# Optimization experiments

Hardware: AMD Instinct MI355X
Metric: run time of the kernel (lower is better)

The kernel has to match this reference:

```python
import jax, jax.numpy as jnp
import numpy as np

B, S, D, H, F, R = 4, 128, 512, 8, 2048, 8
DH = D // H
THRESH = 0.1  # hardcoded in the torch module


def _ln(x, g, b):
    m = x.mean(-1, keepdims=True)
    v = ((x - m) ** 2).mean(-1, keepdims=True)
    return (x - m) * jax.lax.rsqrt(v + 1e-5) * g + b


def setup_inputs() -> dict:
    key = jax.random.key(0)
    ks = jax.random.split(key, 12)
    w = lambda k, shape, std: jax.random.normal(k, shape, jnp.float32) * std
    s = 1.0 / np.sqrt(D)
    qk_std = 2.0 / np.sqrt(D)  # peaky attention so adjacency threshold fires
    return {
        "x": jax.random.normal(ks[0], (B, S, D), jnp.float32),
        "ln1_g": jnp.ones(D, jnp.float32), "ln1_b": jnp.zeros(D, jnp.float32),
        "wq": w(ks[1], (D, D), qk_std), "bq": jnp.zeros(D, jnp.float32),
        "wk": w(ks[2], (D, D), qk_std), "bk": jnp.zeros(D, jnp.float32),
        "wv": w(ks[3], (D, D), s), "bv": jnp.zeros(D, jnp.float32),
        "wo": w(ks[4], (D, D), s), "bo": jnp.zeros(D, jnp.float32),
        "w1": w(ks[5], (D, F), s), "b1": jnp.zeros(F, jnp.float32),
        "w2": w(ks[6], (F, D), 1.0 / np.sqrt(F)), "b2": jnp.zeros(D, jnp.float32),
        "rc_w1": w(ks[7], (2 * D, D), 1.0 / np.sqrt(2 * D)), "rc_b1": jnp.zeros(D, jnp.float32),
        "rc_w2": w(ks[8], (D, R), s), "rc_b2": jnp.zeros(R, jnp.float32),
        "kg_w": w(ks[9], (R, D, D), s),
        "s2n_w": w(ks[10], (D, D), s), "s2n_b": jnp.zeros(D, jnp.float32),
        "ln2_g": jnp.ones(D, jnp.float32), "ln2_b": jnp.zeros(D, jnp.float32),
    }


def reference(x, ln1_g, ln1_b, wq, bq, wk, bk, wv, bv, wo, bo,
              w1, b1, w2, b2, rc_w1, rc_b1, rc_w2, rc_b2,
              kg_w, s2n_w, s2n_b, ln2_g, ln2_b):
    # pre-norm attention
    xn = _ln(x, ln1_g, ln1_b)
    q = (xn @ wq + bq).reshape(B, S, H, DH)
    k = (xn @ wk + bk).reshape(B, S, H, DH)
    v = (xn @ wv + bv).reshape(B, S, H, DH)
    scores = jnp.einsum('bihd,bjhd->bhij', q, k) / np.sqrt(DH)
    attn = jax.nn.softmax(scores, axis=-1)                  # [B,H,S,S]
    ctx = jnp.einsum('bhij,bjhd->bihd', attn, v).reshape(B, S, D)
    attn_out = ctx @ wo + bo
    # FFN -> neural_understanding (no residual, as in source)
    nu = jax.nn.relu(attn_out @ w1 + b1) @ w2 + b2          # [B,S,D]
    # dynamic edge extraction, expressed as a dense mask (jit-safe)
    am = attn.mean(axis=1)                                  # [B,S,S]
    adj = (am > THRESH) & (~jnp.eye(S, dtype=bool))         # u != v
    # relation classifier on every (u,v) pair; mask selects real edges
    a_part = nu @ rc_w1[:D]                                 # concept1 half
    b_part = nu @ rc_w1[D:]                                 # concept2 half
    h = jax.nn.relu(a_part[:, :, None, :] + b_part[:, None, :, :] + rc_b1)  # [B,S,S,D]
    logits = h @ rc_w2 + rc_b2                              # [B,S,S,R]
    pred = jnp.argmax(logits, axis=-1)
    valid = adj & (pred != 0)                               # relation 0 == NONE
    oh = jax.nn.one_hot(pred, R, dtype=nu.dtype) * valid[..., None].astype(nu.dtype)
    # RGCN-style knowledge graph conv: message u -> v with per-relation weight
    transformed = jnp.einsum('bud,rde->bure', nu, kg_w)     # [B,S,R,D]
    agg = jnp.einsum('buvr,bure->bve', oh, transformed)     # [B,S,D]
    reasoned = nu + agg
    neural_result = reasoned @ s2n_w + s2n_b
    out = _ln(x + neural_result, ln2_g, ln2_b)
    return out
```

## Files before the change

kernel.cpp:

```cpp
#include <hip/hip_runtime.h>
#include <hip/hip_bf16.h>

#define B_ 4
#define S_ 128
#define D_ 512
#define H_ 8
#define DH_ 64
#define F_ 2048
#define R_ 8
#define BS_ (B_ * S_)
#define BSD_ (BS_ * D_)
#define E_ 262144

typedef __attribute__((ext_vector_type(8))) short short8;
typedef __attribute__((ext_vector_type(4))) float f32x4;
typedef __attribute__((ext_vector_type(4))) unsigned short ushort4v;

__device__ __forceinline__ void split2(float a, unsigned short& h, unsigned short& l) {
    unsigned u = __float_as_uint(a);
    unsigned hr = (u + 0x7FFFu + ((u >> 16) & 1u)) >> 16;
    h = (unsigned short)hr;
    float lo = a - __uint_as_float(hr << 16);
    unsigned u2 = __float_as_uint(lo);
    l = (unsigned short)((u2 + 0x7FFFu + ((u2 >> 16) & 1u)) >> 16);
}

#define RP 40

struct GemmLds {
    unsigned short A[2][2][64][RP];
    unsigned short B[2][2][64][RP];
};

struct TDesc { const float* s; unsigned short* h; unsigned short* l; int K; int N; int off; };
struct TPack { TDesc d[10]; };

__global__ void prep_kernel(TPack p, int nt, const float* __restrict__ x,
                            const float* __restrict__ g, const float* __restrict__ be,
                            unsigned short* __restrict__ xh, unsigned short* __restrict__ xl) {
    __shared__ float tr[32][33];
    __shared__ float red[256];
    int bid = blockIdx.x;
    if (bid < nt) {
        int wi = 0;
#pragma unroll
        for (int i = 1; i < 10; ++i) if (bid >= p.d[i].off) wi = i;
        const TDesc dd = p.d[wi];
        int t = bid - dd.off;
        int ntk = dd.K / 32;
        int tk = t % ntk, tn = t / ntk;
        int k0 = tk * 32, n0 = tn * 32;
        int col = threadIdx.x & 31, rg = threadIdx.x >> 5;
#pragma unroll
        for (int i = 0; i < 4; ++i) {
            int row = rg * 4 + i;
            tr[row][col] = dd.s[(size_t)(k0 + row) * dd.N + n0 + col];
        }
        __syncthreads();
#pragma unroll
        for (int i = 0; i < 4; ++i) {
            int n = n0 + rg * 4 + i;
            int k = k0 + col;
            unsigned short h, l;
            split2(tr[col][rg * 4 + i], h, l);
            dd.h[(size_t)n * dd.K + k] = h;
            dd.l[(size_t)n * dd.K + k] = l;
        }
    } else {
        int row = bid - nt;
        int t = threadIdx.x;
        const float* xr = x + (size_t)row * D_;
        float v0 = xr[t], v1 = xr[t + 256];
        red[t] = v0 + v1;
        __syncthreads();
        for (int off = 128; off > 0; off >>= 1) { if (t < off) red[t] += red[t + off]; __syncthreads(); }
        float mean = red[0] * (1.0f / D_);
        __syncthreads();
        float d0 = v0 - mean, d1 = v1 - mean;
        red[t] = d0 * d0 + d1 * d1;
        __syncthreads();
        for (int off = 128; off > 0; off >>= 1) { if (t < off) red[t] += red[t + off]; __syncthreads(); }
        float rs = rsqrtf(red[0] * (1.0f / D_) + 1e-5f);
        float o0 = d0 * rs * g[t] + be[t];
        float o1 = d1 * rs * g[t + 256] + be[t + 256];
        unsigned short h, l;
        split2(o0, h, l); xh[(size_t)row * D_ + t] = h;       xl[(size_t)row * D_ + t] = l;
        split2(o1, h, l); xh[(size_t)row * D_ + t + 256] = h; xl[(size_t)row * D_ + t + 256] = l;
    }
}

__device__ __forceinline__ void mgemm_core(const unsigned short* __restrict__ Ath,
                                           const unsigned short* __restrict__ Atl,
                                           const unsigned short* __restrict__ Bth,
                                           const unsigned short* __restrict__ Btl,
                                           int K, int rowBase, int colBase,
                                           int kStart, int nsteps,
                                           f32x4 acc[2][2], GemmLds* L) {
    int tid = threadIdx.x;
    int w = tid >> 6, lane = tid & 63;
    int lm = lane & 15, quad = lane >> 4;
    int wm = (w & 1) * 32, wn = (w >> 1) * 32;
    int rS = tid >> 2, kcS = (tid & 3) * 8;
    size_t aoff = (size_t)(rowBase + rS) * K + kStart + kcS;
    size_t boff = (size_t)(colBase + rS) * K + kStart + kcS;
    short8 rah = *(const short8*)&Ath[aoff];
    short8 ral = *(const short8*)&Atl[aoff];
    short8 rbh = *(const short8*)&Bth[boff];
    short8 rbl = *(const short8*)&Btl[boff];
    for (int s = 0; s < nsteps; ++s) {
        int p = s & 1;
        *(short8*)&L->A[p][0][rS][kcS] = rah;
        *(short8*)&L->A[p][1][rS][kcS] = ral;
        *(short8*)&L->B[p][0][rS][kcS] = rbh;
        *(short8*)&L->B[p][1][rS][kcS] = rbl;
        __syncthreads();
        if (s + 1 < nsteps) {
            size_t ao = aoff + (size_t)(s + 1) * 32;
            size_t bo = boff + (size_t)(s + 1) * 32;
            rah = *(const short8*)&Ath[ao];
            ral = *(const short8*)&Atl[ao];
            rbh = *(const short8*)&Bth[bo];
            rbl = *(const short8*)&Btl[bo];
        }
        short8 ah[2], al[2], bh[2], bl[2];
#pragma unroll
        for (int t = 0; t < 2; ++t) {
            ah[t] = *(const short8*)&L->A[p][0][wm + t * 16 + lm][quad * 8];
            al[t] = *(const short8*)&L->A[p][1][wm + t * 16 + lm][quad * 8];
            bh[t] = *(const short8*)&L->B[p][0][wn + t * 16 + lm][quad * 8];
            bl[t] = *(const short8*)&L->B[p][1][wn + t * 16 + lm][quad * 8];
        }
#pragma unroll
        for (int tm = 0; tm < 2; ++tm)
#pragma unroll
            for (int tn = 0; tn < 2; ++tn) {
                acc[tm][tn] = __builtin_amdgcn_mfma_f32_16x16x32_bf16(ah[tm], bh[tn], acc[tm][tn], 0, 0, 0);
                acc[tm][tn] = __builtin_amdgcn_mfma_f32_16x16x32_bf16(ah[tm], bl[tn], acc[tm][tn], 0, 0, 0);
                acc[tm][tn] = __builtin_amdgcn_mfma_f32_16x16x32_bf16(al[tm], bh[tn], acc[tm][tn], 0, 0, 0);
            }
    }
}

__global__ __launch_bounds__(256) void mgemm_kernel(const unsigned short* __restrict__ Ath,
                                                    const unsigned short* __restrict__ Atl,
                                                    const unsigned short* __restrict__ Bth,
                                                    const unsigned short* __restrict__ Btl,
                                                    const float* __restrict__ bias,
                                                    float* __restrict__ Cf,
                                                    unsigned short* __restrict__ Ch,
                                                    unsigned short* __restrict__ Cl,
                                                    int N, int K, int relu) {
    __shared__ GemmLds L;
    int tid = threadIdx.x;
    int w = tid >> 6, lane = tid & 63;
    int lm = lane & 15, quad = lane >> 4;
    int wm = (w & 1) * 32, wn = (w >> 1) * 32;
    int rowBase = blockIdx.y * 64, colBase = blockIdx.x * 64;
    f32x4 acc[2][2] = {};
    mgemm_core(Ath, Atl, Bth, Btl, K, rowBase, colBase, 0, K / 32, acc, &L);
#pragma unroll
    for (int tm = 0; tm < 2; ++tm)
#pragma unroll
        for (int tn = 0; tn < 2; ++tn) {
            int col = colBase + wn + tn * 16 + lm;
            float bi = bias ? bias[col] : 0.f;
#pragma unroll
            for (int r = 0; r < 4; ++r) {
                int row = rowBase + wm + tm * 16 + quad * 4 + r;
                float v = acc[tm][tn][r] + bi;
                if (relu) v = fmaxf(v, 0.f);
                size_t o = (size_t)row * N + col;
                if (Cf) Cf[o] = v;
                if (Ch) {
                    unsigned short sh, sl;
                    split2(v, sh, sl);
                    Ch[o] = sh; Cl[o] = sl;
                }
            }
        }
}

__global__ __launch_bounds__(256) void mgemm_zw_kernel(const unsigned short* __restrict__ Ath,
                                                       const unsigned short* __restrict__ Atl,
                                                       const unsigned short* __restrict__ Bth,
                                                       const unsigned short* __restrict__ Btl,
                                                       const float* __restrict__ b0,
                                                       const float* __restrict__ b1,
                                                       const float* __restrict__ b2,
                                                       float* __restrict__ Cbase,
                                                       int M, int N, int K) {
    __shared__ GemmLds L;
    int z = blockIdx.z;
    const unsigned short* bth = Bth + (size_t)z * K * N;
    const unsigned short* btl = Btl + (size_t)z * K * N;
    const float* bias = (z == 0) ? b0 : (z == 1) ? b1 : b2;
    float* C = Cbase + (size_t)z * M * N;
    int tid = threadIdx.x;
    int w = tid >> 6, lane = tid & 63;
    int lm = lane & 15, quad = lane >> 4;
    int wm = (w & 1) * 32, wn = (w >> 1) * 32;
    int rowBase = blockIdx.y * 64, colBase = blockIdx.x * 64;
    f32x4 acc[2][2] = {};
    mgemm_core(Ath, Atl, bth, btl, K, rowBase, colBase, 0, K / 32, acc, &L);
#pragma unroll
    for (int tm = 0; tm < 2; ++tm)
#pragma unroll
        for (int tn = 0; tn < 2; ++tn) {
            int col = colBase + wn + tn * 16 + lm;
            float bi = bias ? bias[col] : 0.f;
#pragma unroll
            for (int r = 0; r < 4; ++r) {
                int row = rowBase + wm + tm * 16 + quad * 4 + r;
                C[(size_t)row * N + col] = acc[tm][tn][r] + bi;
            }
        }
}

__global__ __launch_bounds__(256) void mgemm_part_kernel(const unsigned short* __restrict__ Ath,
                                                         const unsigned short* __restrict__ Atl,
                                                         const unsigned short* __restrict__ Bth,
                                                         const unsigned short* __restrict__ Btl,
                                                         float* __restrict__ Cbase,
                                                         int M, int N, int K) {
    __shared__ GemmLds L;
    int ks = gridDim.z, z = blockIdx.z;
    int kLen = K / ks, kStart = z * kLen;
    float* C = Cbase + (size_t)z * M * N;
    int tid = threadIdx.x;
    int w = tid >> 6, lane = tid & 63;
    int lm = lane & 15, quad = lane >> 4;
    int wm = (w & 1) * 32, wn = (w >> 1) * 32;
    int rowBase = blockIdx.y * 64, colBase = blockIdx.x * 64;
    f32x4 acc[2][2] = {};
    mgemm_core(Ath, Atl, Bth, Btl, K, rowBase, colBase, kStart, kLen / 32, acc, &L);
#pragma unroll
    for (int tm = 0; tm < 2; ++tm)
#pragma unroll
        for (int tn = 0; tn < 2; ++tn) {
            int col = colBase + wn + tn * 16 + lm;
#pragma unroll
            for (int r = 0; r < 4; ++r) {
                int row = rowBase + wm + tm * 16 + quad * 4 + r;
                C[(size_t)row * N + col] = acc[tm][tn][r];
            }
        }
}

__global__ void reduce4_kernel(const float* __restrict__ part, const float* __restrict__ b2,
                               float* __restrict__ nu,
                               unsigned short* __restrict__ nh, unsigned short* __restrict__ nl) {
    int base = blockIdx.x * 1024 + threadIdx.x * 4;
    f32x4 s = *(const f32x4*)&b2[base & (D_ - 1)];
#pragma unroll
    for (int z = 0; z < 4; ++z) s += *(const f32x4*)&part[(size_t)z * BSD_ + base];
    *(f32x4*)&nu[base] = s;
    ushort4v hv, lv;
#pragma unroll
    for (int i = 0; i < 4; ++i) { unsigned short h, l; split2(s[i], h, l); hv[i] = h; lv[i] = l; }
    *(ushort4v*)&nh[base] = hv;
    *(ushort4v*)&nl[base] = lv;
}

__global__ void reduce8_kernel(const float* __restrict__ part, const float* __restrict__ nu,
                               unsigned short* __restrict__ rh, unsigned short* __restrict__ rl) {
    int base = blockIdx.x * 1024 + threadIdx.x * 4;
    f32x4 s = *(const f32x4*)&nu[base];
#pragma unroll
    for (int z = 0; z < 8; ++z) s += *(const f32x4*)&part[(size_t)z * BSD_ + base];
    ushort4v hv, lv;
#pragma unroll
    for (int i = 0; i < 4; ++i) { unsigned short h, l; split2(s[i], h, l); hv[i] = h; lv[i] = l; }
    *(ushort4v*)&rh[base] = hv;
    *(ushort4v*)&rl[base] = lv;
}

__global__ __launch_bounds__(512) void attn_fused_kernel(const float* __restrict__ q,
                                                         const float* __restrict__ k,
                                                         const float* __restrict__ v,
                                                         unsigned short* __restrict__ ch,
                                                         unsigned short* __restrict__ cl,
                                                         int* __restrict__ ecount,
                                                         int* __restrict__ elist) {
    __shared__ float qsm[H_][DH_];
    __shared__ float psm[H_][S_];
    int h = threadIdx.x >> 6, lane = threadIdx.x & 63;
    int blk = blockIdx.x;
    int i = blk & (S_ - 1);
    int b = blk >> 7;
    const float* qrow = q + (size_t)(b * S_ + i) * D_ + h * DH_;
    qsm[h][lane] = qrow[lane];
    __syncthreads();
    float s0 = 0.f, s1 = 0.f;
    const float* k0p = k + (size_t)(b * S_ + lane) * D_ + h * DH_;
    const float* k1p = k0p + (size_t)64 * D_;
#pragma unroll 8
    for (int d = 0; d < DH_; ++d) {
        float qd = qsm[h][d];
        s0 += qd * k0p[d];
        s1 += qd * k1p[d];
    }
    s0 *= 0.125f; s1 *= 0.125f;
    float m = fmaxf(s0, s1);
#pragma unroll
    for (int off = 32; off > 0; off >>= 1) m = fmaxf(m, __shfl_xor(m, off));
    float e0 = __expf(s0 - m), e1 = __expf(s1 - m);
    float sum = e0 + e1;
#pragma unroll
    for (int off = 32; off > 0; off >>= 1) sum += __shfl_xor(sum, off);
    float inv = 1.f / sum;
    psm[h][lane] = e0 * inv;
    psm[h][lane + 64] = e1 * inv;
    __syncthreads();
    if (threadIdx.x < S_) {
        int j = threadIdx.x;
        float s = 0.f;
#pragma unroll
        for (int hh = 0; hh < H_; ++hh) s += psm[hh][j];
        s *= (1.0f / H_);
        if (s > 0.1f && i != j) {
            int p = atomicAdd(ecount, 1);
            elist[p] = blk * S_ + j;
        }
    }
    const float* vbase = v + (size_t)b * S_ * D_ + h * DH_ + lane;
    float acc = 0.f;
    for (int j = 0; j < S_; ++j) acc += psm[h][j] * vbase[(size_t)j * D_];
    unsigned short sh, sl;
    split2(acc, sh, sl);
    size_t o = (size_t)(b * S_ + i) * D_ + h * DH_ + lane;
    ch[o] = sh; cl[o] = sl;
}

__global__ __launch_bounds__(64) void edge_kernel(const float* __restrict__ a_part,
                                                  const float* __restrict__ b_part,
                                                  const float* __restrict__ rc_b1,
                                                  const float* __restrict__ rc_w2,
                                                  const float* __restrict__ rc_b2,
                                                  const int* __restrict__ elist,
                                                  const int* __restrict__ ecount,
                                                  int* __restrict__ rel) {
    int lane = threadIdx.x;
    int n = *ecount;
    for (int e = blockIdx.x; e < n; e += gridDim.x) {
        int idx = elist[e];
        int vv = idx & (S_ - 1);
        int bu = idx >> 7;
        int u = bu & (S_ - 1);
        int b = bu >> 7;
        const float* ap = a_part + (size_t)(b * S_ + u) * D_;
        const float* bp = b_part + (size_t)(b * S_ + vv) * D_;
        float lp[R_];
#pragma unroll
        for (int r = 0; r < R_; ++r) lp[r] = 0.f;
#pragma unroll
        for (int jj = 0; jj < D_ / 64; ++jj) {
            int d = lane + jj * 64;
            float hv = fmaxf(ap[d] + bp[d] + rc_b1[d], 0.f);
#pragma unroll
            for (int r = 0; r < R_; ++r) lp[r] += hv * rc_w2[d * R_ + r];
        }
#pragma unroll
        for (int r = 0; r < R_; ++r) {
#pragma unroll
            for (int off = 32; off > 0; off >>= 1) lp[r] += __shfl_down(lp[r], off);
        }
        if (lane == 0) {
            float best = lp[0] + rc_b2[0];
            int bi = 0;
#pragma unroll
            for (int r = 1; r < R_; ++r) {
                float L = lp[r] + rc_b2[r];
                if (L > best) { best = L; bi = r; }
            }
            rel[idx] = bi;
        }
    }
}

__global__ __launch_bounds__(128) void mbuild_kernel(const float* __restrict__ nu,
                                                     const int* __restrict__ rel,
                                                     unsigned short* __restrict__ Mh,
                                                     unsigned short* __restrict__ Ml) {
    __shared__ float acc[R_ * D_];
    __shared__ int rl[S_];
    int blk = blockIdx.x;
    int vv = blk & (S_ - 1);
    int b = blk >> 7;
    int t = threadIdx.x;
    for (int i = t; i < R_ * D_; i += 128) acc[i] = 0.f;
    rl[t] = rel[((size_t)b * S_ + t) * S_ + vv];
    __syncthreads();
    for (int u = 0; u < S_; ++u) {
        int r = rl[u];
        if (r > 0) {
            const float* nurow = nu + (size_t)(b * S_ + u) * D_;
            float* arow = acc + r * D_;
#pragma unroll
            for (int jj = 0; jj < D_ / 128; ++jj) arow[t + jj * 128] += nurow[t + jj * 128];
        }
    }
    __syncthreads();
    unsigned short* Hrow = Mh + (size_t)blk * (R_ * D_);
    unsigned short* Lrow = Ml + (size_t)blk * (R_ * D_);
    for (int i = t; i < R_ * D_; i += 128) {
        unsigned short sh, sl;
        split2(acc[i], sh, sl);
        Hrow[i] = sh; Lrow[i] = sl;
    }
}

__global__ void ln2_kernel(const float* __restrict__ x, const float* __restrict__ y,
                           const float* __restrict__ g, const float* __restrict__ be,
                           float* __restrict__ out) {
    int row = blockIdx.x;
    int t = threadIdx.x;
    __shared__ float red[256];
    float v0 = x[row * D_ + t]       + y[row * D_ + t];
    float v1 = x[row * D_ + t + 256] + y[row * D_ + t + 256];
    red[t] = v0 + v1;
    __syncthreads();
    for (int off = 128; off > 0; off >>= 1) {
        if (t < off) red[t] += red[t + off];
        __syncthreads();
    }
    float mean = red[0] * (1.0f / D_);
    __syncthreads();
    float d0 = v0 - mean, d1 = v1 - mean;
    red[t] = d0 * d0 + d1 * d1;
    __syncthreads();
    for (int off = 128; off > 0; off >>= 1) {
        if (t < off) red[t] += red[t + off];
        __syncthreads();
    }
    float rs = rsqrtf(red[0] * (1.0f / D_) + 1e-5f);
    out[row * D_ + t]       = d0 * rs * g[t]       + be[t];
    out[row * D_ + t + 256] = d1 * rs * g[t + 256] + be[t + 256];
}

extern "C" void kernel_launch(void* const* d_in, const int* in_sizes, int n_in,
                              void* d_out, int out_size, void* d_ws, size_t ws_size,
                              hipStream_t stream) {
    const float* x     = (const float*)d_in[0];
    const float* ln1_g = (const float*)d_in[1];
    const float* ln1_b = (const float*)d_in[2];
    const float* wq    = (const float*)d_in[3];
    const float* bq    = (const float*)d_in[4];
    const float* wk    = (const float*)d_in[5];
    const float* bk    = (const float*)d_in[6];
    const float* wv    = (const float*)d_in[7];
    const float* bv    = (const float*)d_in[8];
    const float* wo    = (const float*)d_in[9];
    const float* bo    = (const float*)d_in[10];
    const float* w1    = (const float*)d_in[11];
    const float* b1    = (const float*)d_in[12];
    const float* w2    = (const float*)d_in[13];
    const float* b2    = (const float*)d_in[14];
    const float* rc_w1 = (const float*)d_in[15];
    const float* rc_b1 = (const float*)d_in[16];
    const float* rc_w2 = (const float*)d_in[17];
    const float* rc_b2 = (const float*)d_in[18];
    const float* kg_w  = (const float*)d_in[19];
    const float* s2n_w = (const float*)d_in[20];
    const float* s2n_b = (const float*)d_in[21];
    const float* ln2_g = (const float*)d_in[22];
    const float* ln2_b = (const float*)d_in[23];
    float* out = (float*)d_out;

    const int BS  = BS_;
    const int BSD = BSD_;

    unsigned short* wt = (unsigned short*)d_ws;
    unsigned short* qkv_h = wt;
    unsigned short* qkv_l = wt + 3 * E_;
    unsigned short* wo_h  = wt + 6 * E_;
    unsigned short* wo_l  = wt + 7 * E_;
    unsigned short* w1_h  = wt + 8 * E_;
    unsigned short* w1_l  = wt + 12 * E_;
    unsigned short* w2_h  = wt + 16 * E_;
    unsigned short* w2_l  = wt + 20 * E_;
    unsigned short* rc_h  = wt + 24 * E_;
    unsigned short* rc_l  = wt + 26 * E_;
    unsigned short* kg_h  = wt + 28 * E_;
    unsigned short* kg_l  = wt + 36 * E_;
    unsigned short* s2_h  = wt + 44 * E_;
    unsigned short* s2_l  = wt + 45 * E_;

    unsigned short* xn_h  = wt + 46 * E_;
    unsigned short* xn_l  = xn_h + BSD;
    unsigned short* ctx_h = xn_l + BSD;
    unsigned short* ctx_l = ctx_h + BSD;
    unsigned short* ao_h  = ctx_l + BSD;
    unsigned short* ao_l  = ao_h + BSD;
    unsigned short* hid_h = ao_l + BSD;
    unsigned short* hid_l = hid_h + (size_t)BS * F_;
    unsigned short* nu_h  = hid_l + (size_t)BS * F_;
    unsigned short* nu_l  = nu_h + BSD;
    unsigned short* mb_h  = nu_l + BSD;
    unsigned short* mb_l  = mb_h + (size_t)BS * R_ * D_;
    unsigned short* rs_h  = mb_l + (size_t)BS * R_ * D_;
    unsigned short* rs_l  = rs_h + BSD;

    float* fbase  = (float*)(rs_l + BSD);
    float* q      = fbase;
    float* v_     = q + 2 * BSD;
    float* apart  = q + 3 * BSD;
    float* nu     = apart + 2 * BSD;
    float* y      = nu + BSD;
    float* part4  = y + BSD;
    float* part8  = part4 + 4 * BSD;

    int* rel    = (int*)(part8 + 8 * BSD);
    int* ecount = rel + B_ * S_ * S_;
    int* elist  = ecount + 64;

    hipMemsetAsync(rel, 0, (size_t)(B_ * S_ * S_ + 64) * 4, stream);
    TPack tp;
    int off = 0;
    auto setd = [&](int i, const float* s, unsigned short* h, unsigned short* l, int K, int N) {
        tp.d[i] = TDesc{s, h, l, K, N, off};
        off += (K / 32) * (N / 32);
    };
    setd(0, wq, qkv_h,          qkv_l,          D_, D_);
    setd(1, wk, qkv_h + E_,     qkv_l + E_,     D_, D_);
    setd(2, wv, qkv_h + 2 * E_, qkv_l + 2 * E_, D_, D_);
    setd(3, wo, wo_h, wo_l, D_, D_);
    setd(4, w1, w1_h, w1_l, D_, F_);
    setd(5, w2, w2_h, w2_l, F_, D_);
    setd(6, rc_w1,            rc_h,      rc_l,      D_, D_);
    setd(7, rc_w1 + D_ * D_,  rc_h + E_, rc_l + E_, D_, D_);
    setd(8, kg_w, kg_h, kg_l, R_ * D_, D_);
    setd(9, s2n_w, s2_h, s2_l, D_, D_);
    hipLaunchKernelGGL(prep_kernel, dim3(off + BS), dim3(256), 0, stream, tp, off,
                       x, ln1_g, ln1_b, xn_h, xn_l);

    hipLaunchKernelGGL(mgemm_zw_kernel, dim3(D_ / 64, BS / 64, 3), dim3(256), 0, stream,
                       xn_h, xn_l, qkv_h, qkv_l, bq, bk, bv, q, BS, D_, D_);
    hipLaunchKernelGGL(attn_fused_kernel, dim3(BS), dim3(512), 0, stream,
                       q, q + BSD, v_, ctx_h, ctx_l, ecount, elist);
    hipLaunchKernelGGL(mgemm_kernel, dim3(D_ / 64, BS / 64), dim3(256), 0, stream,
                       ctx_h, ctx_l, wo_h, wo_l, bo, (float*)nullptr, ao_h, ao_l, D_, D_, 0);
    hipLaunchKernelGGL(mgemm_kernel, dim3(F_ / 64, BS / 64), dim3(256), 0, stream,
                       ao_h, ao_l, w1_h, w1_l, b1, (float*)nullptr, hid_h, hid_l, F_, D_, 1);
    hipLaunchKernelGGL(mgemm_part_kernel, dim3(D_ / 64, BS / 64, 4), dim3(256), 0, stream,
                       hid_h, hid_l, w2_h, w2_l, part4, BS, D_, F_);
    hipLaunchKernelGGL(reduce4_kernel, dim3(BSD / 1024), dim3(256), 0, stream,
                       part4, b2, nu, nu_h, nu_l);
    hipLaunchKernelGGL(mgemm_zw_kernel, dim3(D_ / 64, BS / 64, 2), dim3(256), 0, stream,
                       nu_h, nu_l, rc_h, rc_l, (const float*)nullptr, (const float*)nullptr,
                       (const float*)nullptr, apart, BS, D_, D_);
    hipLaunchKernelGGL(edge_kernel, dim3(256), dim3(64), 0, stream,
                       apart, apart + BSD, rc_b1, rc_w2, rc_b2, elist, ecount, rel);
    hipLaunchKernelGGL(mbuild_kernel, dim3(BS), dim3(128), 0, stream, nu, rel, mb_h, mb_l);
    hipLaunchKernelGGL(mgemm_part_kernel, dim3(D_ / 64, BS / 64, 8), dim3(256), 0, stream,
                       mb_h, mb_l, kg_h, kg_l, part8, BS, D_, R_ * D_);
    hipLaunchKernelGGL(reduce8_kernel, dim3(BSD / 1024), dim3(256), 0, stream,
                       part8, nu, rs_h, rs_l);
    hipLaunchKernelGGL(mgemm_kernel, dim3(D_ / 64, BS / 64), dim3(256), 0, stream,
                       rs_h, rs_l, s2_h, s2_l, s2n_b, y, (unsigned short*)nullptr,
                       (unsigned short*)nullptr, D_, D_, 0);
    hipLaunchKernelGGL(ln2_kernel, dim3(BS), dim3(256), 0, stream, x, y, ln2_g, ln2_b, out);
}
```

Before: 252.5 us.

## Load GEMM fragments directly from global memory and pack four edges per block

Measured after the change: 307.6 us. +21.8%, slower.

```diff
diff --git a/kernel.cpp b/kernel.cpp
--- a/kernel.cpp
+++ b/kernel.cpp
@@ -24,13 +24,6 @@
     unsigned u2 = __float_as_uint(lo);
     l = (unsigned short)((u2 + 0x7FFFu + ((u2 >> 16) & 1u)) >> 16);
 }
-
-#define RP 40
-
-struct GemmLds {
-    unsigned short A[2][2][64][RP];
-    unsigned short B[2][2][64][RP];
-};
 
 struct TDesc { const float* s; unsigned short* h; unsigned short* l; int K; int N; int off; };
 struct TPack { TDesc d[10]; };
@@ -95,40 +88,34 @@
                                            const unsigned short* __restrict__ Btl,
                                            int K, int rowBase, int colBase,
                                            int kStart, int nsteps,
-                                           f32x4 acc[2][2], GemmLds* L) {
+                                           f32x4 acc[2][2]) {
     int tid = threadIdx.x;
     int w = tid >> 6, lane = tid & 63;
     int lm = lane & 15, quad = lane >> 4;
     int wm = (w & 1) * 32, wn = (w >> 1) * 32;
-    int rS = tid >> 2, kcS = (tid & 3) * 8;
-    size_t aoff = (size_t)(rowBase + rS) * K + kStart + kcS;
-    size_t boff = (size_t)(colBase + rS) * K + kStart + kcS;
-    short8 rah = *(const short8*)&Ath[aoff];
-    short8 ral = *(const short8*)&Atl[aoff];
-    short8 rbh = *(const short8*)&Bth[boff];
-    short8 rbl = *(const short8*)&Btl[boff];
+    size_t aoff = (size_t)(rowBase + wm + lm) * K + kStart + quad * 8;
+    size_t boff = (size_t)(colBase + wn + lm) * K + kStart + quad * 8;
+    const size_t rstep = (size_t)16 * K;
+    short8 ah[2], al[2], bh[2], bl[2];
+#pragma unroll
+    for (int t = 0; t < 2; ++t) {
+        ah[t] = *(const short8*)&Ath[aoff + t * rstep];
+        al[t] = *(const short8*)&Atl[aoff + t * rstep];
+        bh[t] = *(const short8*)&Bth[boff + t * rstep];
+        bl[t] = *(const short8*)&Btl[boff + t * rstep];
+    }
     for (int s = 0; s < nsteps; ++s) {
-        int p = s & 1;
-        *(short8*)&L->A[p][0][rS][kcS] = rah;
-        *(short8*)&L->A[p][1][rS][kcS] = ral;
-        *(short8*)&L->B[p][0][rS][kcS] = rbh;
-        *(short8*)&L->B[p][1][rS][kcS] = rbl;
-        __syncthreads();
+        short8 nah[2], nal[2], nbh[2], nbl[2];
         if (s + 1 < nsteps) {
             size_t ao = aoff + (size_t)(s + 1) * 32;
             size_t bo = boff + (size_t)(s + 1) * 32;
-            rah = *(const short8*)&Ath[ao];
-            ral = *(const short8*)&Atl[ao];
-            rbh = *(const short8*)&Bth[bo];
-            rbl = *(const short8*)&Btl[bo];
-        }
-        short8 ah[2], al[2], bh[2], bl[2];
-#pragma unroll
-        for (int t = 0; t < 2; ++t) {
-            ah[t] = *(const short8*)&L->A[p][0][wm + t * 16 + lm][quad * 8];
-            al[t] = *(const short8*)&L->A[p][1][wm + t * 16 + lm][quad * 8];
-            bh[t] = *(const short8*)&L->B[p][0][wn + t * 16 + lm][quad * 8];
-            bl[t] = *(const short8*)&L->B[p][1][wn + t * 16 + lm][quad * 8];
+#pragma unroll
+            for (int t = 0; t < 2; ++t) {
+                nah[t] = *(const short8*)&Ath[ao + t * rstep];
+                nal[t] = *(const short8*)&Atl[ao + t * rstep];
+                nbh[t] = *(const short8*)&Bth[bo + t * rstep];
+                nbl[t] = *(const short8*)&Btl[bo + t * rstep];
+            }
         }
 #pragma unroll
         for (int tm = 0; tm < 2; ++tm)
@@ -138,6 +125,12 @@
                 acc[tm][tn] = __builtin_amdgcn_mfma_f32_16x16x32_bf16(ah[tm], bl[tn], acc[tm][tn], 0, 0, 0);
                 acc[tm][tn] = __builtin_amdgcn_mfma_f32_16x16x32_bf16(al[tm], bh[tn], acc[tm][tn], 0, 0, 0);
             }
+        if (s + 1 < nsteps) {
+#pragma unroll
+            for (int t = 0; t < 2; ++t) {
+                ah[t] = nah[t]; al[t] = nal[t]; bh[t] = nbh[t]; bl[t] = nbl[t];
+            }
+        }
     }
 }
 
@@ -150,14 +143,13 @@
                                                     unsigned short* __restrict__ Ch,
                                                     unsigned short* __restrict__ Cl,
                                                     int N, int K, int relu) {
-    __shared__ GemmLds L;
     int tid = threadIdx.x;
     int w = tid >> 6, lane = tid & 63;
     int lm = lane & 15, quad = lane >> 4;
     int wm = (w & 1) * 32, wn = (w >> 1) * 32;
     int rowBase = blockIdx.y * 64, colBase = blockIdx.x * 64;
     f32x4 acc[2][2] = {};
-    mgemm_core(Ath, Atl, Bth, Btl, K, rowBase, colBase, 0, K / 32, acc, &L);
+    mgemm_core(Ath, Atl, Bth, Btl, K, rowBase, colBase, 0, K / 32, acc);
 #pragma unroll
     for (int tm = 0; tm < 2; ++tm)
 #pragma unroll
@@ -189,7 +181,6 @@
                                                        const float* __restrict__ b2,
                                                        float* __restrict__ Cbase,
                                                        int M, int N, int K) {
-    __shared__ GemmLds L;
     int z = blockIdx.z;
     const unsigned short* bth = Bth + (size_t)z * K * N;
     const unsigned short* btl = Btl + (size_t)z * K * N;
@@ -201,7 +192,7 @@
     int wm = (w & 1) * 32, wn = (w >> 1) * 32;
     int rowBase = blockIdx.y * 64, colBase = blockIdx.x * 64;
     f32x4 acc[2][2] = {};
-    mgemm_core(Ath, Atl, bth, btl, K, rowBase, colBase, 0, K / 32, acc, &L);
+    mgemm_core(Ath, Atl, bth, btl, K, rowBase, colBase, 0, K / 32, acc);
 #pragma unroll
     for (int tm = 0; tm < 2; ++tm)
 #pragma unroll
@@ -222,7 +213,6 @@
                                                          const unsigned short* __restrict__ Btl,
                                                          float* __restrict__ Cbase,
                                                          int M, int N, int K) {
-    __shared__ GemmLds L;
     int ks = gridDim.z, z = blockIdx.z;
     int kLen = K / ks, kStart = z * kLen;
     float* C = Cbase + (size_t)z * M * N;
@@ -232,7 +222,7 @@
     int wm = (w & 1) * 32, wn = (w >> 1) * 32;
     int rowBase = blockIdx.y * 64, colBase = blockIdx.x * 64;
     f32x4 acc[2][2] = {};
-    mgemm_core(Ath, Atl, Bth, Btl, K, rowBase, colBase, kStart, kLen / 32, acc, &L);
+    mgemm_core(Ath, Atl, Bth, Btl, K, rowBase, colBase, kStart, kLen / 32, acc);
 #pragma unroll
     for (int tm = 0; tm < 2; ++tm)
 #pragma unroll
@@ -331,17 +321,17 @@
     ch[o] = sh; cl[o] = sl;
 }
 
-__global__ __launch_bounds__(64) void edge_kernel(const float* __restrict__ a_part,
-                                                  const float* __restrict__ b_part,
-                                                  const float* __restrict__ rc_b1,
-                                                  const float* __restrict__ rc_w2,
-                                                  const float* __restrict__ rc_b2,
-                                                  const int* __restrict__ elist,
-                                                  const int* __restrict__ ecount,
-                                                  int* __restrict__ rel) {
-    int lane = threadIdx.x;
+__global__ __launch_bounds__(256) void edge_kernel(const float* __restrict__ a_part,
+                                                   const float* __restrict__ b_part,
+                                                   const float* __restrict__ rc_b1,
+                                                   const float* __restrict__ rc_w2,
+                                                   const float* __restrict__ rc_b2,
+                                                   const int* __restrict__ elist,
+                                                   const int* __restrict__ ecount,
+                                                   int* __restrict__ rel) {
+    int w = threadIdx.x >> 6, lane = threadIdx.x & 63;
     int n = *ecount;
-    for (int e = blockIdx.x; e < n; e += gridDim.x) {
+    for (int e = blockIdx.x * 4 + w; e < n; e += gridDim.x * 4) {
         int idx = elist[e];
         int vv = idx & (S_ - 1);
         int bu = idx >> 7;
@@ -548,7 +538,7 @@
     hipLaunchKernelGGL(mgemm_zw_kernel, dim3(D_ / 64, BS / 64, 2), dim3(256), 0, stream,
                        nu_h, nu_l, rc_h, rc_l, (const float*)nullptr, (const float*)nullptr,
                        (const float*)nullptr, apart, BS, D_, D_);
-    hipLaunchKernelGGL(edge_kernel, dim3(256), dim3(64), 0, stream,
+    hipLaunchKernelGGL(edge_kernel, dim3(256), dim3(256), 0, stream,
                        apart, apart + BSD, rc_b1, rc_w2, rc_b2, elist, ecount, rel);
     hipLaunchKernelGGL(mbuild_kernel, dim3(BS), dim3(128), 0, stream, nu, rel, mb_h, mb_l);
     hipLaunchKernelGGL(mgemm_part_kernel, dim3(D_ / 64, BS / 64, 8), dim3(256), 0, stream,
```

## Load GEMM tiles directly to LDS and pack four edges per block

Applied to the files above, without the earlier changes.

Measured after the change: 251.3 us. Within noise of the previous version (-0.5%).

```diff
diff --git a/kernel.cpp b/kernel.cpp
--- a/kernel.cpp
+++ b/kernel.cpp
@@ -25,13 +25,6 @@
     l = (unsigned short)((u2 + 0x7FFFu + ((u2 >> 16) & 1u)) >> 16);
 }
 
-#define RP 40
-
-struct GemmLds {
-    unsigned short A[2][2][64][RP];
-    unsigned short B[2][2][64][RP];
-};
-
 struct TDesc { const float* s; unsigned short* h; unsigned short* l; int K; int N; int off; };
 struct TPack { TDesc d[10]; };
 
@@ -87,6 +80,17 @@
         split2(o0, h, l); xh[(size_t)row * D_ + t] = h;       xl[(size_t)row * D_ + t] = l;
         split2(o1, h, l); xh[(size_t)row * D_ + t + 256] = h; xl[(size_t)row * D_ + t + 256] = l;
     }
+}
+
+struct GemmLds {
+    unsigned short A[2][2][64][32];
+    unsigned short B[2][2][64][32];
+};
+
+__device__ __forceinline__ void gload16(const unsigned short* g, unsigned short* l) {
+    __builtin_amdgcn_global_load_lds(
+        (const __attribute__((address_space(1))) void*)g,
+        (__attribute__((address_space(3))) void*)l, 16, 0, 0);
 }
 
 __device__ __forceinline__ void mgemm_core(const unsigned short* __restrict__ Ath,
@@ -101,26 +105,24 @@
     int lm = lane & 15, quad = lane >> 4;
     int wm = (w & 1) * 32, wn = (w >> 1) * 32;
     int rS = tid >> 2, kcS = (tid & 3) * 8;
+    int wb = w * 512;
     size_t aoff = (size_t)(rowBase + rS) * K + kStart + kcS;
     size_t boff = (size_t)(colBase + rS) * K + kStart + kcS;
-    short8 rah = *(const short8*)&Ath[aoff];
-    short8 ral = *(const short8*)&Atl[aoff];
-    short8 rbh = *(const short8*)&Bth[boff];
-    short8 rbl = *(const short8*)&Btl[boff];
+    gload16(&Ath[aoff], &L->A[0][0][0][0] + wb);
+    gload16(&Atl[aoff], &L->A[0][1][0][0] + wb);
+    gload16(&Bth[boff], &L->B[0][0][0][0] + wb);
+    gload16(&Btl[boff], &L->B[0][1][0][0] + wb);
+    __syncthreads();
     for (int s = 0; s < nsteps; ++s) {
         int p = s & 1;
-        *(short8*)&L->A[p][0][rS][kcS] = rah;
-        *(short8*)&L->A[p][1][rS][kcS] = ral;
-        *(short8*)&L->B[p][0][rS][kcS] = rbh;
-        *(short8*)&L->B[p][1][rS][kcS] = rbl;
-        __syncthreads();
         if (s + 1 < nsteps) {
+            int pn = p ^ 1;
             size_t ao = aoff + (size_t)(s + 1) * 32;
             size_t bo = boff + (size_t)(s + 1) * 32;
-            rah = *(const short8*)&Ath[ao];
-            ral = *(const short8*)&Atl[ao];
-            rbh = *(const short8*)&Bth[bo];
-            rbl = *(const short8*)&Btl[bo];
+            gload16(&Ath[ao], &L->A[pn][0][0][0] + wb);
+            gload16(&Atl[ao], &L->A[pn][1][0][0] + wb);
+            gload16(&Bth[bo], &L->B[pn][0][0][0] + wb);
+            gload16(&Btl[bo], &L->B[pn][1][0][0] + wb);
         }
         short8 ah[2], al[2], bh[2], bl[2];
 #pragma unroll
@@ -138,6 +140,7 @@
                 acc[tm][tn] = __builtin_amdgcn_mfma_f32_16x16x32_bf16(ah[tm], bl[tn], acc[tm][tn], 0, 0, 0);
                 acc[tm][tn] = __builtin_amdgcn_mfma_f32_16x16x32_bf16(al[tm], bh[tn], acc[tm][tn], 0, 0, 0);
             }
+        __syncthreads();
     }
 }
 
@@ -331,17 +334,17 @@
     ch[o] = sh; cl[o] = sl;
 }
 
-__global__ __launch_bounds__(64) void edge_kernel(const float* __restrict__ a_part,
-                                                  const float* __restrict__ b_part,
-                                                  const float* __restrict__ rc_b1,
-                                                  const float* __restrict__ rc_w2,
-                                                  const float* __restrict__ rc_b2,
-                                                  const int* __restrict__ elist,
-                                                  const int* __restrict__ ecount,
-                                                  int* __restrict__ rel) {
-    int lane = threadIdx.x;
+__global__ __launch_bounds__(256) void edge_kernel(const float* __restrict__ a_part,
+                                                   const float* __restrict__ b_part,
+                                                   const float* __restrict__ rc_b1,
+                                                   const float* __restrict__ rc_w2,
+                                                   const float* __restrict__ rc_b2,
+                                                   const int* __restrict__ elist,
+                                                   const int* __restrict__ ecount,
+                                                   int* __restrict__ rel) {
+    int w = threadIdx.x >> 6, lane = threadIdx.x & 63;
     int n = *ecount;
-    for (int e = blockIdx.x; e < n; e += gridDim.x) {
+    for (int e = blockIdx.x * 4 + w; e < n; e += gridDim.x * 4) {
         int idx = elist[e];
         int vv = idx & (S_ - 1);
         int bu = idx >> 7;
@@ -548,7 +551,7 @@
     hipLaunchKernelGGL(mgemm_zw_kernel, dim3(D_ / 64, BS / 64, 2), dim3(256), 0, stream,
                        nu_h, nu_l, rc_h, rc_l, (const float*)nullptr, (const float*)nullptr,
                        (const float*)nullptr, apart, BS, D_, D_);
-    hipLaunchKernelGGL(edge_kernel, dim3(256), dim3(64), 0, stream,
+    hipLaunchKernelGGL(edge_kernel, dim3(256), dim3(256), 0, stream,
                        apart, apart + BSD, rc_b1, rc_w2, rc_b2, elist, ecount, rel);
     hipLaunchKernelGGL(mbuild_kernel, dim3(BS), dim3(128), 0, stream, nu, rel, mb_h, mb_l);
     hipLaunchKernelGGL(mgemm_part_kernel, dim3(D_ / 64, BS / 64, 8), dim3(256), 0, stream,
```
